# Kernel optimization log

Measured on AMD Instinct MI355X. Metric: run time of the kernel, lower is better.

## Reference

```python
import jax, jax.numpy as jnp
import numpy as np

N_NODES = 40000
N_EDGES = 640000
D = 128
BN_EPS = 1e-5


def setup_inputs() -> dict:
    key = jax.random.key(0)
    k1, k2, k3, k4 = jax.random.split(key, 4)
    x = jax.random.normal(k1, (N_NODES, D), dtype=jnp.float32)
    edge_index = jax.random.randint(k2, (2, N_EDGES), 0, N_NODES, dtype=jnp.int64)
    W = jax.random.normal(k3, (D, D), dtype=jnp.float32) * (1.0 / np.sqrt(D))
    b = jax.random.normal(k4, (D,), dtype=jnp.float32) * 0.01
    gamma = jnp.ones((D,), dtype=jnp.float32)
    beta = jnp.zeros((D,), dtype=jnp.float32)
    return {"x": x, "edge_index": edge_index, "W": W, "b": b,
            "gamma": gamma, "beta": beta}


def reference(x, edge_index, W, b, gamma, beta):
    num_nodes = x.shape[0]
    # linear projection: [N, D_in] @ [D_in, D_out]
    h = x @ W.T + b
    src, dst = edge_index[0], edge_index[1]
    # gather messages from source nodes, scatter-add into destinations
    msgs = jax.ops.segment_sum(h[src], dst, num_segments=num_nodes)  # [N, D]
    # in-degree of each destination node, clamped to >= 1
    deg = jax.ops.segment_sum(jnp.ones_like(dst, dtype=h.dtype), dst,
                              num_segments=num_nodes)
    deg = jnp.maximum(deg, 1.0)
    h = h + msgs / deg[:, None]
    # BatchNorm1d (training mode: biased batch statistics over nodes)
    mean = jnp.mean(h, axis=0)
    var = jnp.mean(jnp.square(h - mean), axis=0)
    out = (h - mean) * jax.lax.rsqrt(var + BN_EPS) * gamma + beta
    return jax.nn.relu(out)
```

## Files before the change

kernel.cpp:

```cpp
#include <hip/hip_runtime.h>

#define NN 40000
#define NE 640000
#define DD 128
#define MAXDEG 64
#define BN_EPS 1e-5f
#define GEMM_BLKS 313
#define BUCKET_BLKS 320
#define PADK 132
#define POISON 0xAAAAAAAAu

typedef __attribute__((ext_vector_type(8))) short short8;
typedef __attribute__((ext_vector_type(4))) float f32x4;
typedef __attribute__((ext_vector_type(2))) float f32x2;

__device__ __forceinline__ unsigned int rb16(float x) {
  unsigned int u = __float_as_uint(x);
  return (u + 0x7fffu + ((u >> 16) & 1u)) >> 16;
}

__global__ __launch_bounds__(256) void fat_kernel(
    const float* __restrict__ x, const float* __restrict__ W,
    const float* __restrict__ bias, unsigned int* __restrict__ hbf,
    unsigned int* __restrict__ hfp8, const int* __restrict__ ei,
    unsigned int* __restrict__ cursors, unsigned short* __restrict__ esorted) {
  __shared__ unsigned short xs[128 * PADK];
  const int tid = threadIdx.x;

  if (blockIdx.x >= GEMM_BLKS) {
    const int b = blockIdx.x - GEMM_BLKS;
    for (int e = b * 256 + tid; e < NE; e += BUCKET_BLKS * 256) {
      const int s = ei[e];
      const int d = ei[NE + e];
      const unsigned p = atomicAdd(&cursors[d], 1u) - POISON;
      if (p < MAXDEG) esorted[d * MAXDEG + p] = (unsigned short)s;
    }
    return;
  }

  const int node0 = blockIdx.x * 128;
#pragma unroll
  for (int it = 0; it < 16; ++it) {
    const int flat = it * 256 + tid;
    const int row = flat >> 5;
    const int c4 = flat & 31;
    const int gn = node0 + row;
    float4 v = make_float4(0.f, 0.f, 0.f, 0.f);
    if (gn < NN) v = *reinterpret_cast<const float4*>(x + (size_t)gn * DD + c4 * 4);
    ushort4 p;
    p.x = (unsigned short)rb16(v.x);
    p.y = (unsigned short)rb16(v.y);
    p.z = (unsigned short)rb16(v.z);
    p.w = (unsigned short)rb16(v.w);
    *reinterpret_cast<ushort4*>(&xs[row * PADK + c4 * 4]) = p;
  }
  __syncthreads();

  const int wave = tid >> 6;
  const int lane = tid & 63;
  const int m = lane & 15;
  const int g = lane >> 4;
  f32x4 acc[2][8];
#pragma unroll
  for (int t = 0; t < 2; ++t)
#pragma unroll
    for (int ct = 0; ct < 8; ++ct) acc[t][ct] = (f32x4){0.f, 0.f, 0.f, 0.f};

#pragma unroll
  for (int ks = 0; ks < 4; ++ks) {
    const int ko = ks * 32 + g * 8;
    short8 a[2], b[8];
#pragma unroll
    for (int t = 0; t < 2; ++t)
      a[t] = *reinterpret_cast<const short8*>(&xs[(wave * 32 + t * 16 + m) * PADK + ko]);
#pragma unroll
    for (int ct = 0; ct < 8; ++ct) {
      const float* wr = W + (size_t)(ct * 16 + m) * DD + ko;
      const float4 w0 = *reinterpret_cast<const float4*>(wr);
      const float4 w1 = *reinterpret_cast<const float4*>(wr + 4);
      short8 bb;
      bb[0] = (short)rb16(w0.x);
      bb[1] = (short)rb16(w0.y);
      bb[2] = (short)rb16(w0.z);
      bb[3] = (short)rb16(w0.w);
      bb[4] = (short)rb16(w1.x);
      bb[5] = (short)rb16(w1.y);
      bb[6] = (short)rb16(w1.z);
      bb[7] = (short)rb16(w1.w);
      b[ct] = bb;
    }
#pragma unroll
    for (int t = 0; t < 2; ++t)
#pragma unroll
      for (int ct = 0; ct < 8; ++ct)
        acc[t][ct] = __builtin_amdgcn_mfma_f32_16x16x32_bf16(a[t], b[ct], acc[t][ct], 0, 0, 0);
  }
  __syncthreads();

#pragma unroll
  for (int t = 0; t < 2; ++t) {
#pragma unroll
    for (int ct = 0; ct < 8; ++ct) {
      const int ch = ct * 16 + m;
      const float bv = bias[ch];
#pragma unroll
      for (int reg = 0; reg < 4; ++reg) {
        const int nrow = wave * 32 + t * 16 + g * 4 + reg;
        xs[nrow * PADK + ch] = (unsigned short)rb16(acc[t][ct][reg] + bv);
      }
    }
  }
  __syncthreads();
#pragma unroll
  for (int it = 0; it < 8; ++it) {
    const int flat = it * 256 + tid;
    const int row = flat >> 4;
    const int c8 = flat & 15;
    const int gn = node0 + row;
    if (gn < NN) {
      const uint4 o = *reinterpret_cast<const uint4*>(&xs[row * PADK + c8 * 8]);
      *reinterpret_cast<uint4*>(hbf + (size_t)gn * 64 + c8 * 4) = o;
      const float f0 = __uint_as_float(o.x << 16);
      const float f1 = __uint_as_float(o.x & 0xffff0000u);
      const float f2 = __uint_as_float(o.y << 16);
      const float f3 = __uint_as_float(o.y & 0xffff0000u);
      const float f4 = __uint_as_float(o.z << 16);
      const float f5 = __uint_as_float(o.z & 0xffff0000u);
      const float f6 = __uint_as_float(o.w << 16);
      const float f7 = __uint_as_float(o.w & 0xffff0000u);
      int r0 = __builtin_amdgcn_cvt_pk_fp8_f32(f0, f1, 0, false);
      r0 = __builtin_amdgcn_cvt_pk_fp8_f32(f2, f3, r0, true);
      int r1 = __builtin_amdgcn_cvt_pk_fp8_f32(f4, f5, 0, false);
      r1 = __builtin_amdgcn_cvt_pk_fp8_f32(f6, f7, r1, true);
      *reinterpret_cast<uint2*>(hfp8 + (size_t)gn * 32 + c8 * 2) =
          make_uint2((unsigned)r0, (unsigned)r1);
    }
  }
}

__global__ __launch_bounds__(256) void gather_kernel(
    const unsigned int* __restrict__ hbf, const unsigned int* __restrict__ hfp8,
    const unsigned short* __restrict__ esorted,
    const unsigned int* __restrict__ cursors, float* __restrict__ v_out,
    float* __restrict__ sums) {
  const int tid = threadIdx.x;
  const int wv = tid >> 6;
  const int lane = tid & 63;
  const int q = lane >> 4;
  const int c = lane & 15;
  const int nW = gridDim.x * 4;
  const int wid = blockIdx.x * 4 + wv;
  float s8[8], q8[8];
#pragma unroll
  for (int j = 0; j < 8; ++j) { s8[j] = 0.f; q8[j] = 0.f; }

  int n = wid;
  int deg = 0, sraw = 0;
  uint4 su = make_uint4(0u, 0u, 0u, 0u);
  if (n < NN) {
    deg = (int)(cursors[n] - POISON);
    sraw = (int)esorted[n * MAXDEG + lane];
    su = *reinterpret_cast<const uint4*>(hbf + (size_t)n * 64 + c * 4);
  }
  while (n < NN) {
    const int n2 = n + nW;
    int deg2 = 0, sraw2 = 0;
    uint4 su2 = make_uint4(0u, 0u, 0u, 0u);
    if (n2 < NN) {
      deg2 = (int)(cursors[n2] - POISON);
      sraw2 = (int)esorted[n2 * MAXDEG + lane];
      su2 = *reinterpret_cast<const uint4*>(hbf + (size_t)n2 * 64 + c * 4);
    }
    const int dcl = min(deg, MAXDEG);
    float acc[8];
#pragma unroll
    for (int j = 0; j < 8; ++j) acc[j] = 0.f;
    for (int i0 = 0; i0 < dcl; i0 += 16) {
      int id[4];
      float w[4];
#pragma unroll
      for (int j = 0; j < 4; ++j) {
        const int e = i0 + q + 4 * j;
        const int idv = __shfl(sraw, min(e, MAXDEG - 1), 64);
        const bool vld = e < dcl;
        id[j] = vld ? idv : n;
        w[j] = vld ? 1.f : 0.f;
      }
#pragma unroll
      for (int j = 0; j < 4; ++j) {
        const uint2 u =
            *reinterpret_cast<const uint2*>(hfp8 + (size_t)id[j] * 32 + c * 2);
        const f32x2 p01 = __builtin_amdgcn_cvt_pk_f32_fp8(u.x, false);
        const f32x2 p23 = __builtin_amdgcn_cvt_pk_f32_fp8(u.x, true);
        const f32x2 p45 = __builtin_amdgcn_cvt_pk_f32_fp8(u.y, false);
        const f32x2 p67 = __builtin_amdgcn_cvt_pk_f32_fp8(u.y, true);
        acc[0] = fmaf(p01.x, w[j], acc[0]);
        acc[1] = fmaf(p01.y, w[j], acc[1]);
        acc[2] = fmaf(p23.x, w[j], acc[2]);
        acc[3] = fmaf(p23.y, w[j], acc[3]);
        acc[4] = fmaf(p45.x, w[j], acc[4]);
        acc[5] = fmaf(p45.y, w[j], acc[5]);
        acc[6] = fmaf(p67.x, w[j], acc[6]);
        acc[7] = fmaf(p67.y, w[j], acc[7]);
      }
    }
#pragma unroll
    for (int j = 0; j < 8; ++j) {
      acc[j] += __shfl_xor(acc[j], 16, 64);
      acc[j] += __shfl_xor(acc[j], 32, 64);
    }
    if (q == 0) {
      const float rdeg = 1.0f / (float)max(deg, 1);
      float v[8];
      v[0] = __uint_as_float(su.x << 16) + acc[0] * rdeg;
      v[1] = __uint_as_float(su.x & 0xffff0000u) + acc[1] * rdeg;
      v[2] = __uint_as_float(su.y << 16) + acc[2] * rdeg;
      v[3] = __uint_as_float(su.y & 0xffff0000u) + acc[3] * rdeg;
      v[4] = __uint_as_float(su.z << 16) + acc[4] * rdeg;
      v[5] = __uint_as_float(su.z & 0xffff0000u) + acc[5] * rdeg;
      v[6] = __uint_as_float(su.w << 16) + acc[6] * rdeg;
      v[7] = __uint_as_float(su.w & 0xffff0000u) + acc[7] * rdeg;
      *reinterpret_cast<float4*>(v_out + (size_t)n * DD + c * 8) =
          make_float4(v[0], v[1], v[2], v[3]);
      *reinterpret_cast<float4*>(v_out + (size_t)n * DD + c * 8 + 4) =
          make_float4(v[4], v[5], v[6], v[7]);
#pragma unroll
      for (int j = 0; j < 8; ++j) {
        s8[j] += v[j];
        q8[j] += v[j] * v[j];
      }
    }
    n = n2;
    deg = deg2;
    sraw = sraw2;
    su = su2;
  }
  __shared__ float redS[4][128];
  __shared__ float redQ[4][128];
  if (q == 0) {
#pragma unroll
    for (int j = 0; j < 8; ++j) {
      redS[wv][c * 8 + j] = s8[j];
      redQ[wv][c * 8 + j] = q8[j];
    }
  }
  __syncthreads();
  if (tid < 128) {
    const float S = redS[0][tid] + redS[1][tid] + redS[2][tid] + redS[3][tid];
    const float Q = redQ[0][tid] + redQ[1][tid] + redQ[2][tid] + redQ[3][tid];
    const int r = blockIdx.x & 7;
    unsafeAtomicAdd(&sums[r * 256 + tid], S);
    unsafeAtomicAdd(&sums[r * 256 + 128 + tid], Q);
  }
}

__global__ __launch_bounds__(256) void normalize_kernel(
    const float* __restrict__ sums, const float* __restrict__ gamma,
    const float* __restrict__ beta, float* __restrict__ out) {
  __shared__ float sc[128];
  __shared__ float sh[128];
  const int tid = threadIdx.x;
  if (tid < 128) {
    float S = 0.f, Q = 0.f;
#pragma unroll
    for (int r = 0; r < 8; ++r) {
      S += sums[r * 256 + tid];
      Q += sums[r * 256 + 128 + tid];
    }
    const float inv_n = 1.0f / (float)NN;
    const float mean = S * inv_n;
    const float var = Q * inv_n - mean * mean;
    const float inv = rsqrtf(var + BN_EPS);
    const float g = gamma[tid] * inv;
    sc[tid] = g;
    sh[tid] = beta[tid] - mean * g;
  }
  __syncthreads();
  const long total4 = (long)NN * DD / 4;
  for (long i = blockIdx.x * 256L + tid; i < total4; i += (long)gridDim.x * 256L) {
    const int c4 = (int)(i & 31);
    const float4 v = *reinterpret_cast<const float4*>(out + i * 4);
    const float4 scv = *reinterpret_cast<const float4*>(&sc[c4 * 4]);
    const float4 shv = *reinterpret_cast<const float4*>(&sh[c4 * 4]);
    float4 o;
    o.x = fmaxf(v.x * scv.x + shv.x, 0.f);
    o.y = fmaxf(v.y * scv.y + shv.y, 0.f);
    o.z = fmaxf(v.z * scv.z + shv.z, 0.f);
    o.w = fmaxf(v.w * scv.w + shv.w, 0.f);
    *reinterpret_cast<float4*>(out + i * 4) = o;
  }
}

extern "C" void kernel_launch(void* const* d_in, const int* in_sizes, int n_in,
                              void* d_out, int out_size, void* d_ws, size_t ws_size,
                              hipStream_t stream) {
  const float* x     = (const float*)d_in[0];
  const int*   ei    = (const int*)d_in[1];
  const float* W     = (const float*)d_in[2];
  const float* b     = (const float*)d_in[3];
  const float* gamma = (const float*)d_in[4];
  const float* beta  = (const float*)d_in[5];
  float* out = (float*)d_out;

  unsigned int*   hbf     = (unsigned int*)d_ws;
  unsigned int*   hfp8    = hbf + (size_t)NN * 64;
  unsigned short* esorted = (unsigned short*)(hfp8 + (size_t)NN * 32);
  unsigned int*   cursors = (unsigned int*)(esorted + (size_t)NN * MAXDEG);
  float*          sums    = (float*)(cursors + NN);

  fat_kernel<<<GEMM_BLKS + BUCKET_BLKS, 256, 0, stream>>>(
      x, W, b, hbf, hfp8, ei, cursors, esorted);
  gather_kernel<<<2560, 256, 0, stream>>>(hbf, hfp8, esorted, cursors, out, sums);
  normalize_kernel<<<1280, 256, 0, stream>>>(sums, gamma, beta, out);
}
```

Baseline: 139.2 us.

## Replace per-edge global atomics with two-level bucketed edge sort via shared memory

Edge bucketing now counts edges per 128-node bucket in shared memory, reserves bucket ranges with one global atomic per bucket per block, and writes packed (src,dst) pairs into coarse buckets. A new place_kernel then builds per-node adjacency lists with shared-memory atomics and writes them out coalesced, along with byte-packed degrees. This removes 640k scattered global atomics and scattered 2-byte writes, at the cost of an extra kernel launch and an intermediate bucket buffer with a fixed capacity that can overflow.

```diff
diff --git a/kernel.cpp b/kernel.cpp
--- a/kernel.cpp
+++ b/kernel.cpp
@@ -6,7 +6,12 @@
 #define MAXDEG 64
 #define BN_EPS 1e-5f
 #define GEMM_BLKS 313
-#define BUCKET_BLKS 320
+#define BUCKET_BLKS 128
+#define CHUNKA 5000
+#define EPT 20
+#define NBKT 313
+#define NPB 128
+#define CAP 2432
 #define PADK 132
 #define POISON 0xAAAAAAAAu
 
@@ -23,21 +28,46 @@
     const float* __restrict__ x, const float* __restrict__ W,
     const float* __restrict__ bias, unsigned int* __restrict__ hbf,
     unsigned int* __restrict__ hfp8, const int* __restrict__ ei,
-    unsigned int* __restrict__ cursors, unsigned short* __restrict__ esorted) {
-  __shared__ unsigned short xs[128 * PADK];
+    unsigned int* __restrict__ gcur, unsigned int* __restrict__ ebkt) {
+  __shared__ unsigned int smem[128 * PADK / 2];
   const int tid = threadIdx.x;
 
   if (blockIdx.x >= GEMM_BLKS) {
+    unsigned int* cnts = smem;
     const int b = blockIdx.x - GEMM_BLKS;
-    for (int e = b * 256 + tid; e < NE; e += BUCKET_BLKS * 256) {
-      const int s = ei[e];
-      const int d = ei[NE + e];
-      const unsigned p = atomicAdd(&cursors[d], 1u) - POISON;
-      if (p < MAXDEG) esorted[d * MAXDEG + p] = (unsigned short)s;
+    for (int i = tid; i < NBKT; i += 256) cnts[i] = 0u;
+    __syncthreads();
+    const int e0 = b * CHUNKA;
+    unsigned pk[EPT];
+#pragma unroll
+    for (int j = 0; j < EPT; ++j) {
+      const int i = tid + j * 256;
+      if (i < CHUNKA) {
+        const unsigned s = (unsigned)ei[e0 + i];
+        const unsigned d = (unsigned)ei[NE + e0 + i];
+        pk[j] = s | (d << 16);
+        atomicAdd(&cnts[d >> 7], 1u);
+      }
+    }
+    __syncthreads();
+    for (int k = tid; k < NBKT; k += 256) {
+      const unsigned c = cnts[k];
+      cnts[k] = atomicAdd(&gcur[k], c) - POISON;
+    }
+    __syncthreads();
+#pragma unroll
+    for (int j = 0; j < EPT; ++j) {
+      const int i = tid + j * 256;
+      if (i < CHUNKA) {
+        const unsigned d = pk[j] >> 16;
+        const unsigned pos = atomicAdd(&cnts[d >> 7], 1u);
+        if (pos < CAP) ebkt[(size_t)(d >> 7) * CAP + pos] = pk[j];
+      }
     }
     return;
   }
 
+  unsigned short* xs = (unsigned short*)smem;
   const int node0 = blockIdx.x * 128;
 #pragma unroll
   for (int it = 0; it < 16; ++it) {
@@ -138,10 +168,48 @@
   }
 }
 
+__global__ __launch_bounds__(256) void place_kernel(
+    const unsigned int* __restrict__ ebkt, const unsigned int* __restrict__ gcur,
+    unsigned short* __restrict__ esorted, unsigned int* __restrict__ deg32) {
+  __shared__ unsigned int lcur[NPB];
+  __shared__ unsigned short stag[NPB * MAXDEG];
+  const int tid = threadIdx.x;
+  const int k = blockIdx.x;
+  for (int i = tid; i < NPB; i += 256) lcur[i] = 0u;
+  __syncthreads();
+  int total = (int)(gcur[k] - POISON);
+  total = min(total, CAP);
+  const unsigned int* eb = ebkt + (size_t)k * CAP;
+  for (int i = tid; i < total; i += 256) {
+    const unsigned pkv = eb[i];
+    const unsigned ld = (pkv >> 16) & (NPB - 1);
+    const unsigned pos = atomicAdd(&lcur[ld], 1u);
+    if (pos < MAXDEG) stag[ld * MAXDEG + pos] = (unsigned short)(pkv & 0xffffu);
+  }
+  __syncthreads();
+  const int node0 = k * NPB;
+#pragma unroll
+  for (int it = 0; it < 4; ++it) {
+    const int flat = it * 256 + tid;
+    const int row = flat >> 3;
+    const int c = flat & 7;
+    const int gn = node0 + row;
+    if (gn < NN)
+      *reinterpret_cast<uint4*>(esorted + (size_t)gn * MAXDEG + c * 8) =
+          *reinterpret_cast<const uint4*>(&stag[row * MAXDEG + c * 8]);
+  }
+  if (tid < NPB / 4) {
+    unsigned dv = 0;
+#pragma unroll
+    for (int z = 0; z < 4; ++z) dv |= min(lcur[tid * 4 + z], 255u) << (z * 8);
+    deg32[(size_t)node0 / 4 + tid] = dv;
+  }
+}
+
 __global__ __launch_bounds__(256) void gather_kernel(
     const unsigned int* __restrict__ hbf, const unsigned int* __restrict__ hfp8,
     const unsigned short* __restrict__ esorted,
-    const unsigned int* __restrict__ cursors, float* __restrict__ v_out,
+    const unsigned char* __restrict__ deg8, float* __restrict__ v_out,
     float* __restrict__ sums) {
   const int tid = threadIdx.x;
   const int wv = tid >> 6;
@@ -158,7 +226,7 @@
   int deg = 0, sraw = 0;
   uint4 su = make_uint4(0u, 0u, 0u, 0u);
   if (n < NN) {
-    deg = (int)(cursors[n] - POISON);
+    deg = (int)deg8[n];
     sraw = (int)esorted[n * MAXDEG + lane];
     su = *reinterpret_cast<const uint4*>(hbf + (size_t)n * 64 + c * 4);
   }
@@ -167,7 +235,7 @@
     int deg2 = 0, sraw2 = 0;
     uint4 su2 = make_uint4(0u, 0u, 0u, 0u);
     if (n2 < NN) {
-      deg2 = (int)(cursors[n2] - POISON);
+      deg2 = (int)deg8[n2];
       sraw2 = (int)esorted[n2 * MAXDEG + lane];
       su2 = *reinterpret_cast<const uint4*>(hbf + (size_t)n2 * 64 + c * 4);
     }
@@ -305,11 +373,15 @@
   unsigned int*   hbf     = (unsigned int*)d_ws;
   unsigned int*   hfp8    = hbf + (size_t)NN * 64;
   unsigned short* esorted = (unsigned short*)(hfp8 + (size_t)NN * 32);
-  unsigned int*   cursors = (unsigned int*)(esorted + (size_t)NN * MAXDEG);
-  float*          sums    = (float*)(cursors + NN);
+  unsigned int*   ebkt    = (unsigned int*)(esorted + (size_t)NN * MAXDEG);
+  unsigned int*   gcur    = ebkt + (size_t)NBKT * CAP;
+  unsigned int*   deg32   = gcur + NBKT;
+  float*          sums    = (float*)(deg32 + 10016);
 
   fat_kernel<<<GEMM_BLKS + BUCKET_BLKS, 256, 0, stream>>>(
-      x, W, b, hbf, hfp8, ei, cursors, esorted);
-  gather_kernel<<<2560, 256, 0, stream>>>(hbf, hfp8, esorted, cursors, out, sums);
+      x, W, b, hbf, hfp8, ei, gcur, ebkt);
+  place_kernel<<<NBKT, 256, 0, stream>>>(ebkt, gcur, esorted, deg32);
+  gather_kernel<<<2560, 256, 0, stream>>>(hbf, hfp8, esorted,
+                                          (const unsigned char*)deg32, out, sums);
   normalize_kernel<<<1280, 256, 0, stream>>>(sums, gamma, beta, out);
 }
```

New measurement: 141.2 us. No clear change (+1.4%).
